# Performance work log

Hardware: AMD Instinct MI355X
Metric: run time of the kernel (lower is better)

The kernel has to match this reference:

```python
import jax, jax.numpy as jnp
import numpy as np

N_NODES = 50000
N_EDGES = 800000
D_IN, D_HID, D_OUT = 128, 256, 128


def setup_inputs() -> dict:
    key = jax.random.key(0)
    ks = jax.random.split(key, 8)
    x = jax.random.normal(ks[0], (N_NODES, D_IN), dtype=jnp.float32)
    edge_index = jax.random.randint(ks[1], (2, N_EDGES), 0, N_NODES, dtype=jnp.int64)
    # Xavier-ish scale for stability
    W_l1 = jax.random.normal(ks[2], (D_HID, D_IN), dtype=jnp.float32) * (1.0 / np.sqrt(D_IN))
    b_l1 = jnp.zeros((D_HID,), dtype=jnp.float32)
    W_r1 = jax.random.normal(ks[3], (D_HID, D_IN), dtype=jnp.float32) * (1.0 / np.sqrt(D_IN))
    W_l2 = jax.random.normal(ks[4], (D_OUT, D_HID), dtype=jnp.float32) * (1.0 / np.sqrt(D_HID))
    b_l2 = jnp.zeros((D_OUT,), dtype=jnp.float32)
    W_r2 = jax.random.normal(ks[5], (D_OUT, D_HID), dtype=jnp.float32) * (1.0 / np.sqrt(D_HID))
    return {"x": x, "edge_index": edge_index, "W_l1": W_l1, "b_l1": b_l1,
            "W_r1": W_r1, "W_l2": W_l2, "b_l2": b_l2, "W_r2": W_r2}


def _sage_conv(x, src, dst, W_l, b_l, W_r):
    # SAGEConv (aggr='mean', root_weight=True, normalize=False):
    #   out_i = W_l @ mean_{j in N(i)} x_j + b_l + W_r @ x_i
    n = x.shape[0]
    msgs = x[src]                                             # [E, d] gather
    agg = jax.ops.segment_sum(msgs, dst, num_segments=n)      # [N, d] scatter-add
    deg = jax.ops.segment_sum(jnp.ones((src.shape[0],), x.dtype), dst,
                              num_segments=n)
    agg = agg / jnp.maximum(deg, 1.0)[:, None]                # mean (0 for isolated)
    return agg @ W_l.T + b_l + x @ W_r.T


def reference(x, edge_index, W_l1, b_l1, W_r1, W_l2, b_l2, W_r2):
    # Note: PyG BasicGNN with num_layers=1 and jk=None applies NO activation
    # after its single conv, so the stack is two bare SAGEConv layers.
    src, dst = edge_index[0], edge_index[1]
    h = _sage_conv(x, src, dst, W_l1, b_l1, W_r1)
    out = _sage_conv(h, src, dst, W_l2, b_l2, W_r2)
    return out
```

## Files before the change

kernel.cpp:

```cpp
#include <hip/hip_runtime.h>

typedef __attribute__((ext_vector_type(4))) float f32x4;
typedef __attribute__((ext_vector_type(8))) short bf16x8;

__device__ inline ushort f2bf(float f) {
    uint u = __builtin_bit_cast(uint, f);
    u += 0x7fff + ((u >> 16) & 1);
    return (ushort)(u >> 16);
}
__device__ inline float bf2f(ushort h) {
    uint u = ((uint)h) << 16;
    return __builtin_bit_cast(float, u);
}
__device__ inline uint packbf(float lo, float hi) {
    return (uint)f2bf(lo) | ((uint)f2bf(hi) << 16);
}

#define GRP 8
#define NSLICE 6250
#define CHUNK 2048

__global__ __launch_bounds__(256) void k_pre(
    const float* __restrict__ x,
    const float* __restrict__ Wl1, const float* __restrict__ Wr1,
    const float* __restrict__ Wl2, const float* __restrict__ Wr2,
    const int* __restrict__ ei,
    ushort* __restrict__ A1, ushort* __restrict__ W1cat, ushort* __restrict__ W2cat,
    int* __restrict__ cnt, int n, int nE, int nxb, int histBase)
{
    const int b = blockIdx.x;
    if (b < nxb) {
        int e4 = b * 256 + threadIdx.x;
        if (e4 >= n * 32) return;
        int i = e4 >> 5, c4 = e4 & 31;
        float4 v = *(const float4*)(x + (size_t)i * 128 + c4 * 4);
        ushort4 o;
        o.x = f2bf(v.x); o.y = f2bf(v.y); o.z = f2bf(v.z); o.w = f2bf(v.w);
        *(ushort4*)(A1 + (size_t)i * 256 + 128 + c4 * 4) = o;
        return;
    }
    if (b < nxb + 128) {
        int t = (b - nxb) * 256 + threadIdx.x;
        int which = t >> 14;
        int r = (t >> 6) & 255;
        int kq = t & 63;
        const float* src;
        ushort* dst;
        if (which == 0) {
            src = (kq < 32) ? (Wl1 + (size_t)r * 128 + kq * 4)
                            : (Wr1 + (size_t)r * 128 + (kq - 32) * 4);
            dst = W1cat + (size_t)r * 256 + kq * 4;
        } else {
            src = (r < 128) ? (Wl2 + (size_t)r * 256 + kq * 4)
                            : (Wr2 + (size_t)(r - 128) * 256 + kq * 4);
            dst = W2cat + (size_t)r * 256 + kq * 4;
        }
        float4 v = *(const float4*)src;
        ushort4 o;
        o.x = f2bf(v.x); o.y = f2bf(v.y); o.z = f2bf(v.z); o.w = f2bf(v.w);
        *(ushort4*)dst = o;
        return;
    }
    if (b < histBase) return;
    const int hb = b - histBase;
    const int g = hb & 7;
    const int c = hb >> 3;
    const int lo = g * NSLICE, hi = lo + NSLICE;
    #pragma unroll
    for (int p = 0; p < CHUNK / 256; ++p) {
        int e = c * CHUNK + p * 256 + threadIdx.x;
        if (e < nE) {
            int d = ei[nE + e];
            if (d >= lo && d < hi) atomicAdd(&cnt[d], 1);
        }
    }
}

__global__ __launch_bounds__(1024) void k_scan1(const int* __restrict__ cnt,
                                                int* __restrict__ rp,
                                                int* __restrict__ bsum, int n) {
    __shared__ int buf[1024];
    const int tid = threadIdx.x;
    const int i = blockIdx.x * 1024 + tid;
    int v = (i < n) ? cnt[i] : 0;
    buf[tid] = v;
    __syncthreads();
    #pragma unroll
    for (int off = 1; off < 1024; off <<= 1) {
        int t = 0;
        if (tid >= off) t = buf[tid - off];
        __syncthreads();
        if (tid >= off) buf[tid] += t;
        __syncthreads();
    }
    if (i < n) rp[i] = buf[tid] - v;
    if (tid == 1023) bsum[blockIdx.x] = buf[1023];
}

__global__ __launch_bounds__(1024) void k_scan3b(int* __restrict__ rp,
                                                 const int* __restrict__ bsum,
                                                 int nb, int n) {
    __shared__ int sofs;
    if (threadIdx.x < 64) {
        int i = threadIdx.x;
        int v = (i < nb) ? bsum[i] : 0;
        int s = v;
        #pragma unroll
        for (int off = 1; off < 64; off <<= 1) {
            int t = __shfl_up(s, off, 64);
            if (i >= off) s += t;
        }
        if (i == (int)blockIdx.x) sofs = s - v;
        if ((int)blockIdx.x == nb - 1 && i == nb - 1) rp[n] = s;
    }
    __syncthreads();
    int i = blockIdx.x * 1024 + threadIdx.x;
    if (i < n) rp[i] += sofs;
}

__global__ __launch_bounds__(256) void k_fill_p(const int* __restrict__ ei,
                                                const int* __restrict__ rp,
                                                int* __restrict__ cur,
                                                int* __restrict__ srt, int nE) {
    const int g = blockIdx.x & 7;
    const int c = blockIdx.x >> 3;
    const int lo = g * NSLICE, hi = lo + NSLICE;
    #pragma unroll
    for (int p = 0; p < CHUNK / 256; ++p) {
        int e = c * CHUNK + p * 256 + threadIdx.x;
        if (e < nE) {
            int d = ei[nE + e];
            if (d >= lo && d < hi) {
                int s = ei[e];
                int pos = rp[d] + atomicAdd(&cur[d], 1);
                srt[pos] = s;
            }
        }
    }
}

__global__ __launch_bounds__(256) void k_gather1(ushort* A1,
                                                 const int* __restrict__ srt,
                                                 const int* __restrict__ rp, int n) {
    const int node = blockIdx.x * 4 + (threadIdx.x >> 6);
    if (node >= n) return;
    const int lane = threadIdx.x & 63;
    const int quad = lane >> 4;
    const int col16 = (lane & 15) * 16;
    const int beg = rp[node], end = rp[node + 1];
    float a0 = 0.f, a1 = 0.f, a2 = 0.f, a3 = 0.f;
    float a4 = 0.f, a5 = 0.f, a6 = 0.f, a7 = 0.f;
    for (int e = beg; e < end; e += 16) {
        uint4 v[4]; int live[4];
        #pragma unroll
        for (int q = 0; q < 4; ++q) {
            int idx = e + q * 4 + quad;
            live[q] = idx < end;
            int s = srt[live[q] ? idx : end - 1];
            v[q] = *(const uint4*)((const char*)A1 + (size_t)s * 512 + 256 + col16);
        }
        #pragma unroll
        for (int q = 0; q < 4; ++q) {
            if (live[q]) {
                a0 += bf2f((ushort)v[q].x);  a1 += bf2f((ushort)(v[q].x >> 16));
                a2 += bf2f((ushort)v[q].y);  a3 += bf2f((ushort)(v[q].y >> 16));
                a4 += bf2f((ushort)v[q].z);  a5 += bf2f((ushort)(v[q].z >> 16));
                a6 += bf2f((ushort)v[q].w);  a7 += bf2f((ushort)(v[q].w >> 16));
            }
        }
    }
    a0 += __shfl_xor(a0, 16); a1 += __shfl_xor(a1, 16);
    a2 += __shfl_xor(a2, 16); a3 += __shfl_xor(a3, 16);
    a4 += __shfl_xor(a4, 16); a5 += __shfl_xor(a5, 16);
    a6 += __shfl_xor(a6, 16); a7 += __shfl_xor(a7, 16);
    a0 += __shfl_xor(a0, 32); a1 += __shfl_xor(a1, 32);
    a2 += __shfl_xor(a2, 32); a3 += __shfl_xor(a3, 32);
    a4 += __shfl_xor(a4, 32); a5 += __shfl_xor(a5, 32);
    a6 += __shfl_xor(a6, 32); a7 += __shfl_xor(a7, 32);
    if (quad == 0) {
        const float invd = 1.0f / fmaxf((float)(end - beg), 1.0f);
        uint4 o;
        o.x = packbf(a0 * invd, a1 * invd);
        o.y = packbf(a2 * invd, a3 * invd);
        o.z = packbf(a4 * invd, a5 * invd);
        o.w = packbf(a6 * invd, a7 * invd);
        *(uint4*)((char*)A1 + (size_t)node * 512 + col16) = o;
    }
}

__global__ __launch_bounds__(256) void k_gather2(const ushort* __restrict__ H2,
                                                 const int* __restrict__ srt,
                                                 const int* __restrict__ rp,
                                                 const float* __restrict__ b2,
                                                 float* __restrict__ out, int n) {
    const int node = blockIdx.x * 4 + (threadIdx.x >> 6);
    if (node >= n) return;
    const int lane = threadIdx.x & 63;
    const int quad = lane >> 4;
    const int col16 = (lane & 15) * 16;
    const int beg = rp[node], end = rp[node + 1];
    float a0 = 0.f, a1 = 0.f, a2 = 0.f, a3 = 0.f;
    float a4 = 0.f, a5 = 0.f, a6 = 0.f, a7 = 0.f;
    for (int e = beg; e < end; e += 16) {
        uint4 v[4]; int live[4];
        #pragma unroll
        for (int q = 0; q < 4; ++q) {
            int idx = e + q * 4 + quad;
            live[q] = idx < end;
            int s = srt[live[q] ? idx : end - 1];
            v[q] = *(const uint4*)((const char*)H2 + (size_t)s * 512 + col16);
        }
        #pragma unroll
        for (int q = 0; q < 4; ++q) {
            if (live[q]) {
                a0 += bf2f((ushort)v[q].x);  a1 += bf2f((ushort)(v[q].x >> 16));
                a2 += bf2f((ushort)v[q].y);  a3 += bf2f((ushort)(v[q].y >> 16));
                a4 += bf2f((ushort)v[q].z);  a5 += bf2f((ushort)(v[q].z >> 16));
                a6 += bf2f((ushort)v[q].w);  a7 += bf2f((ushort)(v[q].w >> 16));
            }
        }
    }
    a0 += __shfl_xor(a0, 16); a1 += __shfl_xor(a1, 16);
    a2 += __shfl_xor(a2, 16); a3 += __shfl_xor(a3, 16);
    a4 += __shfl_xor(a4, 16); a5 += __shfl_xor(a5, 16);
    a6 += __shfl_xor(a6, 16); a7 += __shfl_xor(a7, 16);
    a0 += __shfl_xor(a0, 32); a1 += __shfl_xor(a1, 32);
    a2 += __shfl_xor(a2, 32); a3 += __shfl_xor(a3, 32);
    a4 += __shfl_xor(a4, 32); a5 += __shfl_xor(a5, 32);
    a6 += __shfl_xor(a6, 32); a7 += __shfl_xor(a7, 32);
    if (quad == 0) {
        const float invd = 1.0f / fmaxf((float)(end - beg), 1.0f);
        uint4 rv = *(const uint4*)((const char*)H2 + (size_t)node * 512 + 256 + col16);
        const int c8 = (lane & 15) * 8;
        float4 bb0 = *(const float4*)(b2 + c8);
        float4 bb1 = *(const float4*)(b2 + c8 + 4);
        float4 r0, r1;
        r0.x = a0 * invd + bf2f((ushort)rv.x) + bb0.x;
        r0.y = a1 * invd + bf2f((ushort)(rv.x >> 16)) + bb0.y;
        r0.z = a2 * invd + bf2f((ushort)rv.y) + bb0.z;
        r0.w = a3 * invd + bf2f((ushort)(rv.y >> 16)) + bb0.w;
        r1.x = a4 * invd + bf2f((ushort)rv.z) + bb1.x;
        r1.y = a5 * invd + bf2f((ushort)(rv.z >> 16)) + bb1.y;
        r1.z = a6 * invd + bf2f((ushort)rv.w) + bb1.z;
        r1.w = a7 * invd + bf2f((ushort)(rv.w >> 16)) + bb1.w;
        *(float4*)(out + (size_t)node * 128 + c8) = r0;
        *(float4*)(out + (size_t)node * 128 + c8 + 4) = r1;
    }
}

__global__ __launch_bounds__(512, 6) void k_gemm_fused(
    const ushort* __restrict__ A, const ushort* __restrict__ W1,
    const ushort* __restrict__ W2, const float* __restrict__ b1,
    ushort* __restrict__ O, int n)
{
    __shared__ __align__(16) char sA[32768];
    const int bi = blockIdx.x * 64;
    const int tid = threadIdx.x;

    #pragma unroll
    for (int p = 0; p < 4; ++p) {
        const int o = p * 8192 + tid * 16;
        const int row = o >> 9;
        const int cb = o & 511;
        uint4 v = *(const uint4*)((const char*)A + (size_t)(bi + row) * 512 + cb);
        *(uint4*)(sA + row * 512 + (cb ^ ((row & 7) << 4))) = v;
    }
    __syncthreads();

    const int wid = tid >> 6;
    const int lane = tid & 63;
    const int wn = wid * 32;
    const int lr = lane & 15;
    const int lkb = (lane >> 4) * 16;
    const int crow0 = (lane >> 4) * 4;
    const int ccol = lane & 15;

    f32x4 acc[4][2] = {};
    #pragma unroll
    for (int kk = 0; kk < 8; ++kk) {
        bf16x8 wf[2], af[4];
        #pragma unroll
        for (int ni = 0; ni < 2; ++ni)
            wf[ni] = *(const bf16x8*)((const char*)W1 + (size_t)(wn + ni * 16 + lr) * 512 + kk * 64 + lkb);
        #pragma unroll
        for (int mi = 0; mi < 4; ++mi) {
            const int row = mi * 16 + lr;
            af[mi] = *(const bf16x8*)(sA + row * 512 + ((kk * 64 + lkb) ^ ((row & 7) << 4)));
        }
        #pragma unroll
        for (int mi = 0; mi < 4; ++mi)
            #pragma unroll
            for (int ni = 0; ni < 2; ++ni)
                acc[mi][ni] = __builtin_amdgcn_mfma_f32_16x16x32_bf16(
                    af[mi], wf[ni], acc[mi][ni], 0, 0, 0);
    }
    __syncthreads();

    {
        const float badd0 = b1[wn + ccol];
        const float badd1 = b1[wn + 16 + ccol];
        #pragma unroll
        for (int mi = 0; mi < 4; ++mi)
            #pragma unroll
            for (int ni = 0; ni < 2; ++ni) {
                const int col = wn + ni * 16 + ccol;
                const float badd = ni ? badd1 : badd0;
                #pragma unroll
                for (int j = 0; j < 4; ++j) {
                    const int row = mi * 16 + crow0 + j;
                    *(ushort*)(sA + row * 512 + ((col * 2) ^ ((row & 7) << 4))) =
                        f2bf(acc[mi][ni][j] + badd);
                }
            }
    }
    __syncthreads();

    {
        f32x4 acc2[4][2] = {};
        #pragma unroll
        for (int kk = 0; kk < 8; ++kk) {
            bf16x8 wf[2], af[4];
            #pragma unroll
            for (int ni = 0; ni < 2; ++ni)
                wf[ni] = *(const bf16x8*)((const char*)W2 + (size_t)(wn + ni * 16 + lr) * 512 + kk * 64 + lkb);
            #pragma unroll
            for (int mi = 0; mi < 4; ++mi) {
                const int row = mi * 16 + lr;
                af[mi] = *(const bf16x8*)(sA + row * 512 + ((kk * 64 + lkb) ^ ((row & 7) << 4)));
            }
            #pragma unroll
            for (int mi = 0; mi < 4; ++mi)
                #pragma unroll
                for (int ni = 0; ni < 2; ++ni)
                    acc2[mi][ni] = __builtin_amdgcn_mfma_f32_16x16x32_bf16(
                        af[mi], wf[ni], acc2[mi][ni], 0, 0, 0);
        }
        #pragma unroll
        for (int mi = 0; mi < 4; ++mi)
            #pragma unroll
            for (int ni = 0; ni < 2; ++ni) {
                const int ocol = wn + ni * 16 + ccol;
                #pragma unroll
                for (int j = 0; j < 4; ++j) {
                    const int grow = bi + mi * 16 + crow0 + j;
                    if (grow < n)
                        O[(size_t)grow * 256 + ocol] = f2bf(acc2[mi][ni][j]);
                }
            }
    }
}

extern "C" void kernel_launch(void* const* d_in, const int* in_sizes, int n_in,
                              void* d_out, int out_size, void* d_ws, size_t ws_size,
                              hipStream_t stream) {
    const float* x   = (const float*)d_in[0];
    const int*   ei  = (const int*)  d_in[1];
    const float* Wl1 = (const float*)d_in[2];
    const float* bl1 = (const float*)d_in[3];
    const float* Wr1 = (const float*)d_in[4];
    const float* Wl2 = (const float*)d_in[5];
    const float* bl2 = (const float*)d_in[6];
    const float* Wr2 = (const float*)d_in[7];
    float* out = (float*)d_out;

    const int nN = 50000;
    const int nE = in_sizes[1] / 2;

    char* ws = (char*)d_ws;
    int*    rp    = (int*)   (ws);
    int*    cnt   = (int*)   (ws + 262144);
    int*    cur   = (int*)   (ws + 524288);
    int*    bsum  = (int*)   (ws + 786432);
    int*    srt   = (int*)   (ws + (size_t)1 * (1 << 20));
    ushort* W1cat = (ushort*)(ws + (size_t)5 * (1 << 20));
    ushort* W2cat = (ushort*)(ws + (size_t)5 * (1 << 20) + 262144);
    ushort* A1    = (ushort*)(ws + (size_t)6 * (1 << 20));
    ushort* H2    = (ushort*)(ws + (size_t)32 * (1 << 20));

    const int nb = (nN + 1023) / 1024;
    const int nChunks = (nE + CHUNK - 1) / CHUNK;
    const int nxb = (nN * 32 + 255) / 256;
    const int histBase = (nxb + 128 + 7) & ~7;

    hipMemsetAsync(cnt, 0, 524288, stream);

    k_pre<<<histBase + nChunks * GRP, 256, 0, stream>>>(
        x, Wl1, Wr1, Wl2, Wr2, ei, A1, W1cat, W2cat, cnt, nN, nE, nxb, histBase);

    k_scan1<<<nb, 1024, 0, stream>>>(cnt, rp, bsum, nN);
    k_scan3b<<<nb, 1024, 0, stream>>>(rp, bsum, nb, nN);
    k_fill_p<<<nChunks * GRP, 256, 0, stream>>>(ei, rp, cur, srt, nE);

    k_gather1<<<(nN + 3) / 4, 256, 0, stream>>>(A1, srt, rp, nN);
    k_gemm_fused<<<(nN + 63) / 64, 512, 0, stream>>>(A1, W1cat, W2cat, bl1, H2, nN);
    k_gather2<<<(nN + 3) / 4, 256, 0, stream>>>(H2, srt, rp, bl2, out, nN);
}
```

Before: 269.7 us.

## Fuse layer-1 neighbor gather into the fused GEMM kernel and split outputs

The first-layer mean aggregation is now done inside the GEMM kernel. Each block gathers neighbor rows for its 64 nodes straight into shared memory, which removes the separate gather kernel and the round trip of the aggregated half of A1 through global memory. The bf16 copy of x is stored compactly (128 columns) and the second GEMM's outputs go to separate T2 and Rb buffers, so gathers read denser rows. W1 and W2 fragments are preloaded into registers, which raises register pressure; the launch_bounds occupancy hint is dropped and the gather runs at lower parallelism, only 8 waves per 64 nodes.

```diff
diff --git a/kernel.cpp b/kernel.cpp
--- a/kernel.cpp
+++ b/kernel.cpp
@@ -25,7 +25,7 @@
     const float* __restrict__ Wl1, const float* __restrict__ Wr1,
     const float* __restrict__ Wl2, const float* __restrict__ Wr2,
     const int* __restrict__ ei,
-    ushort* __restrict__ A1, ushort* __restrict__ W1cat, ushort* __restrict__ W2cat,
+    ushort* __restrict__ A1x, ushort* __restrict__ W1cat, ushort* __restrict__ W2cat,
     int* __restrict__ cnt, int n, int nE, int nxb, int histBase)
 {
     const int b = blockIdx.x;
@@ -36,7 +36,7 @@
         float4 v = *(const float4*)(x + (size_t)i * 128 + c4 * 4);
         ushort4 o;
         o.x = f2bf(v.x); o.y = f2bf(v.y); o.z = f2bf(v.z); o.w = f2bf(v.w);
-        *(ushort4*)(A1 + (size_t)i * 256 + 128 + c4 * 4) = o;
+        *(ushort4*)(A1x + (size_t)i * 128 + c4 * 4) = o;
         return;
     }
     if (b < nxb + 128) {
@@ -139,56 +139,170 @@
     }
 }
 
-__global__ __launch_bounds__(256) void k_gather1(ushort* A1,
-                                                 const int* __restrict__ srt,
-                                                 const int* __restrict__ rp, int n) {
-    const int node = blockIdx.x * 4 + (threadIdx.x >> 6);
-    if (node >= n) return;
-    const int lane = threadIdx.x & 63;
+__global__ __launch_bounds__(512) void k_gemm_fused(
+    const ushort* __restrict__ A1x, const ushort* __restrict__ W1,
+    const ushort* __restrict__ W2, const float* __restrict__ b1,
+    const int* __restrict__ srt, const int* __restrict__ rp,
+    ushort* __restrict__ T2, ushort* __restrict__ Rb, int n)
+{
+    __shared__ __align__(16) char sA[32768];
+    const int bi = blockIdx.x * 64;
+    const int tid = threadIdx.x;
+    const int wid = tid >> 6;
+    const int lane = tid & 63;
+    const int wn = wid * 32;
+    const int lr = lane & 15;
+    const int lkb = (lane >> 4) * 16;
     const int quad = lane >> 4;
     const int col16 = (lane & 15) * 16;
-    const int beg = rp[node], end = rp[node + 1];
-    float a0 = 0.f, a1 = 0.f, a2 = 0.f, a3 = 0.f;
-    float a4 = 0.f, a5 = 0.f, a6 = 0.f, a7 = 0.f;
-    for (int e = beg; e < end; e += 16) {
-        uint4 v[4]; int live[4];
-        #pragma unroll
-        for (int q = 0; q < 4; ++q) {
-            int idx = e + q * 4 + quad;
-            live[q] = idx < end;
-            int s = srt[live[q] ? idx : end - 1];
-            v[q] = *(const uint4*)((const char*)A1 + (size_t)s * 512 + 256 + col16);
-        }
-        #pragma unroll
-        for (int q = 0; q < 4; ++q) {
-            if (live[q]) {
-                a0 += bf2f((ushort)v[q].x);  a1 += bf2f((ushort)(v[q].x >> 16));
-                a2 += bf2f((ushort)v[q].y);  a3 += bf2f((ushort)(v[q].y >> 16));
-                a4 += bf2f((ushort)v[q].z);  a5 += bf2f((ushort)(v[q].z >> 16));
-                a6 += bf2f((ushort)v[q].w);  a7 += bf2f((ushort)(v[q].w >> 16));
-            }
-        }
-    }
-    a0 += __shfl_xor(a0, 16); a1 += __shfl_xor(a1, 16);
-    a2 += __shfl_xor(a2, 16); a3 += __shfl_xor(a3, 16);
-    a4 += __shfl_xor(a4, 16); a5 += __shfl_xor(a5, 16);
-    a6 += __shfl_xor(a6, 16); a7 += __shfl_xor(a7, 16);
-    a0 += __shfl_xor(a0, 32); a1 += __shfl_xor(a1, 32);
-    a2 += __shfl_xor(a2, 32); a3 += __shfl_xor(a3, 32);
-    a4 += __shfl_xor(a4, 32); a5 += __shfl_xor(a5, 32);
-    a6 += __shfl_xor(a6, 32); a7 += __shfl_xor(a7, 32);
-    if (quad == 0) {
-        const float invd = 1.0f / fmaxf((float)(end - beg), 1.0f);
-        uint4 o;
-        o.x = packbf(a0 * invd, a1 * invd);
-        o.y = packbf(a2 * invd, a3 * invd);
-        o.z = packbf(a4 * invd, a5 * invd);
-        o.w = packbf(a6 * invd, a7 * invd);
-        *(uint4*)((char*)A1 + (size_t)node * 512 + col16) = o;
-    }
-}
-
-__global__ __launch_bounds__(256) void k_gather2(const ushort* __restrict__ H2,
+
+    bf16x8 w1r[16];
+    #pragma unroll
+    for (int kk = 0; kk < 8; ++kk)
+        #pragma unroll
+        for (int ni = 0; ni < 2; ++ni)
+            w1r[kk * 2 + ni] = *(const bf16x8*)((const char*)W1 +
+                (size_t)(wn + ni * 16 + lr) * 512 + kk * 64 + lkb);
+
+    #pragma unroll
+    for (int p = 0; p < 2; ++p) {
+        const int idx = p * 512 + tid;
+        const int row = idx >> 4;
+        const int cb = (idx & 15) * 16;
+        uint4 v = *(const uint4*)((const char*)A1x + (size_t)(bi + row) * 256 + cb);
+        *(uint4*)(sA + row * 512 + ((256 + cb) ^ ((row & 7) << 4))) = v;
+    }
+
+    #pragma unroll 1
+    for (int i = 0; i < 8; ++i) {
+        const int row = wid * 8 + i;
+        const int node = bi + row;
+        if (node >= n) continue;
+        const int beg = rp[node], end = rp[node + 1];
+        float a0 = 0.f, a1 = 0.f, a2 = 0.f, a3 = 0.f;
+        float a4 = 0.f, a5 = 0.f, a6 = 0.f, a7 = 0.f;
+        for (int e = beg; e < end; e += 16) {
+            uint4 v[4]; int live[4];
+            #pragma unroll
+            for (int q = 0; q < 4; ++q) {
+                int idx = e + q * 4 + quad;
+                live[q] = idx < end;
+                int s = srt[live[q] ? idx : end - 1];
+                v[q] = *(const uint4*)((const char*)A1x + (size_t)s * 256 + col16);
+            }
+            #pragma unroll
+            for (int q = 0; q < 4; ++q) {
+                if (live[q]) {
+                    a0 += bf2f((ushort)v[q].x);  a1 += bf2f((ushort)(v[q].x >> 16));
+                    a2 += bf2f((ushort)v[q].y);  a3 += bf2f((ushort)(v[q].y >> 16));
+                    a4 += bf2f((ushort)v[q].z);  a5 += bf2f((ushort)(v[q].z >> 16));
+                    a6 += bf2f((ushort)v[q].w);  a7 += bf2f((ushort)(v[q].w >> 16));
+                }
+            }
+        }
+        a0 += __shfl_xor(a0, 16); a1 += __shfl_xor(a1, 16);
+        a2 += __shfl_xor(a2, 16); a3 += __shfl_xor(a3, 16);
+        a4 += __shfl_xor(a4, 16); a5 += __shfl_xor(a5, 16);
+        a6 += __shfl_xor(a6, 16); a7 += __shfl_xor(a7, 16);
+        a0 += __shfl_xor(a0, 32); a1 += __shfl_xor(a1, 32);
+        a2 += __shfl_xor(a2, 32); a3 += __shfl_xor(a3, 32);
+        a4 += __shfl_xor(a4, 32); a5 += __shfl_xor(a5, 32);
+        a6 += __shfl_xor(a6, 32); a7 += __shfl_xor(a7, 32);
+        if (quad == 0) {
+            const float invd = 1.0f / fmaxf((float)(end - beg), 1.0f);
+            uint4 o;
+            o.x = packbf(a0 * invd, a1 * invd);
+            o.y = packbf(a2 * invd, a3 * invd);
+            o.z = packbf(a4 * invd, a5 * invd);
+            o.w = packbf(a6 * invd, a7 * invd);
+            *(uint4*)(sA + row * 512 + (col16 ^ ((row & 7) << 4))) = o;
+        }
+    }
+    __syncthreads();
+
+    const int crow0 = (lane >> 4) * 4;
+    const int ccol = lane & 15;
+
+    f32x4 acc[4][2] = {};
+    {
+        bf16x8 w2r[16];
+        #pragma unroll
+        for (int kk = 0; kk < 8; ++kk)
+            #pragma unroll
+            for (int ni = 0; ni < 2; ++ni)
+                w2r[kk * 2 + ni] = *(const bf16x8*)((const char*)W2 +
+                    (size_t)(wn + ni * 16 + lr) * 512 + kk * 64 + lkb);
+
+        #pragma unroll
+        for (int kk = 0; kk < 8; ++kk) {
+            bf16x8 af[4];
+            #pragma unroll
+            for (int mi = 0; mi < 4; ++mi) {
+                const int row = mi * 16 + lr;
+                af[mi] = *(const bf16x8*)(sA + row * 512 + ((kk * 64 + lkb) ^ ((row & 7) << 4)));
+            }
+            #pragma unroll
+            for (int mi = 0; mi < 4; ++mi)
+                #pragma unroll
+                for (int ni = 0; ni < 2; ++ni)
+                    acc[mi][ni] = __builtin_amdgcn_mfma_f32_16x16x32_bf16(
+                        af[mi], w1r[kk * 2 + ni], acc[mi][ni], 0, 0, 0);
+        }
+        __syncthreads();
+
+        {
+            const float badd0 = b1[wn + ccol];
+            const float badd1 = b1[wn + 16 + ccol];
+            #pragma unroll
+            for (int mi = 0; mi < 4; ++mi)
+                #pragma unroll
+                for (int ni = 0; ni < 2; ++ni) {
+                    const int col = wn + ni * 16 + ccol;
+                    const float badd = ni ? badd1 : badd0;
+                    #pragma unroll
+                    for (int j = 0; j < 4; ++j) {
+                        const int row = mi * 16 + crow0 + j;
+                        *(ushort*)(sA + row * 512 + ((col * 2) ^ ((row & 7) << 4))) =
+                            f2bf(acc[mi][ni][j] + badd);
+                    }
+                }
+        }
+        __syncthreads();
+
+        f32x4 acc2[4][2] = {};
+        #pragma unroll
+        for (int kk = 0; kk < 8; ++kk) {
+            bf16x8 af[4];
+            #pragma unroll
+            for (int mi = 0; mi < 4; ++mi) {
+                const int row = mi * 16 + lr;
+                af[mi] = *(const bf16x8*)(sA + row * 512 + ((kk * 64 + lkb) ^ ((row & 7) << 4)));
+            }
+            #pragma unroll
+            for (int mi = 0; mi < 4; ++mi)
+                #pragma unroll
+                for (int ni = 0; ni < 2; ++ni)
+                    acc2[mi][ni] = __builtin_amdgcn_mfma_f32_16x16x32_bf16(
+                        af[mi], w2r[kk * 2 + ni], acc2[mi][ni], 0, 0, 0);
+        }
+        #pragma unroll
+        for (int mi = 0; mi < 4; ++mi)
+            #pragma unroll
+            for (int ni = 0; ni < 2; ++ni) {
+                const int ocol = wn + ni * 16 + ccol;
+                ushort* dstbase = (ocol < 128) ? (T2 + ocol) : (Rb + ocol - 128);
+                #pragma unroll
+                for (int j = 0; j < 4; ++j) {
+                    const int grow = bi + mi * 16 + crow0 + j;
+                    if (grow < n)
+                        dstbase[(size_t)grow * 128] = f2bf(acc2[mi][ni][j]);
+                }
+            }
+    }
+}
+
+__global__ __launch_bounds__(256) void k_gather2(const ushort* __restrict__ T2,
+                                                 const ushort* __restrict__ Rb,
                                                  const int* __restrict__ srt,
                                                  const int* __restrict__ rp,
                                                  const float* __restrict__ b2,
@@ -208,7 +322,7 @@
             int idx = e + q * 4 + quad;
             live[q] = idx < end;
             int s = srt[live[q] ? idx : end - 1];
-            v[q] = *(const uint4*)((const char*)H2 + (size_t)s * 512 + col16);
+            v[q] = *(const uint4*)((const char*)T2 + (size_t)s * 256 + col16);
         }
         #pragma unroll
         for (int q = 0; q < 4; ++q) {
@@ -230,7 +344,7 @@
     a6 += __shfl_xor(a6, 32); a7 += __shfl_xor(a7, 32);
     if (quad == 0) {
         const float invd = 1.0f / fmaxf((float)(end - beg), 1.0f);
-        uint4 rv = *(const uint4*)((const char*)H2 + (size_t)node * 512 + 256 + col16);
+        uint4 rv = *(const uint4*)((const char*)Rb + (size_t)node * 256 + col16);
         const int c8 = (lane & 15) * 8;
         float4 bb0 = *(const float4*)(b2 + c8);
         float4 bb1 = *(const float4*)(b2 + c8 + 4);
@@ -248,108 +362,6 @@
     }
 }
 
-__global__ __launch_bounds__(512, 6) void k_gemm_fused(
-    const ushort* __restrict__ A, const ushort* __restrict__ W1,
-    const ushort* __restrict__ W2, const float* __restrict__ b1,
-    ushort* __restrict__ O, int n)
-{
-    __shared__ __align__(16) char sA[32768];
-    const int bi = blockIdx.x * 64;
-    const int tid = threadIdx.x;
-
-    #pragma unroll
-    for (int p = 0; p < 4; ++p) {
-        const int o = p * 8192 + tid * 16;
-        const int row = o >> 9;
-        const int cb = o & 511;
-        uint4 v = *(const uint4*)((const char*)A + (size_t)(bi + row) * 512 + cb);
-        *(uint4*)(sA + row * 512 + (cb ^ ((row & 7) << 4))) = v;
-    }
-    __syncthreads();
-
-    const int wid = tid >> 6;
-    const int lane = tid & 63;
-    const int wn = wid * 32;
-    const int lr = lane & 15;
-    const int lkb = (lane >> 4) * 16;
-    const int crow0 = (lane >> 4) * 4;
-    const int ccol = lane & 15;
-
-    f32x4 acc[4][2] = {};
-    #pragma unroll
-    for (int kk = 0; kk < 8; ++kk) {
-        bf16x8 wf[2], af[4];
-        #pragma unroll
-        for (int ni = 0; ni < 2; ++ni)
-            wf[ni] = *(const bf16x8*)((const char*)W1 + (size_t)(wn + ni * 16 + lr) * 512 + kk * 64 + lkb);
-        #pragma unroll
-        for (int mi = 0; mi < 4; ++mi) {
-            const int row = mi * 16 + lr;
-            af[mi] = *(const bf16x8*)(sA + row * 512 + ((kk * 64 + lkb) ^ ((row & 7) << 4)));
-        }
-        #pragma unroll
-        for (int mi = 0; mi < 4; ++mi)
-            #pragma unroll
-            for (int ni = 0; ni < 2; ++ni)
-                acc[mi][ni] = __builtin_amdgcn_mfma_f32_16x16x32_bf16(
-                    af[mi], wf[ni], acc[mi][ni], 0, 0, 0);
-    }
-    __syncthreads();
-
-    {
-        const float badd0 = b1[wn + ccol];
-        const float badd1 = b1[wn + 16 + ccol];
-        #pragma unroll
-        for (int mi = 0; mi < 4; ++mi)
-            #pragma unroll
-            for (int ni = 0; ni < 2; ++ni) {
-                const int col = wn + ni * 16 + ccol;
-                const float badd = ni ? badd1 : badd0;
-                #pragma unroll
-                for (int j = 0; j < 4; ++j) {
-                    const int row = mi * 16 + crow0 + j;
-                    *(ushort*)(sA + row * 512 + ((col * 2) ^ ((row & 7) << 4))) =
-                        f2bf(acc[mi][ni][j] + badd);
-                }
-            }
-    }
-    __syncthreads();
-
-    {
-        f32x4 acc2[4][2] = {};
-        #pragma unroll
-        for (int kk = 0; kk < 8; ++kk) {
-            bf16x8 wf[2], af[4];
-            #pragma unroll
-            for (int ni = 0; ni < 2; ++ni)
-                wf[ni] = *(const bf16x8*)((const char*)W2 + (size_t)(wn + ni * 16 + lr) * 512 + kk * 64 + lkb);
-            #pragma unroll
-            for (int mi = 0; mi < 4; ++mi) {
-                const int row = mi * 16 + lr;
-                af[mi] = *(const bf16x8*)(sA + row * 512 + ((kk * 64 + lkb) ^ ((row & 7) << 4)));
-            }
-            #pragma unroll
-            for (int mi = 0; mi < 4; ++mi)
-                #pragma unroll
-                for (int ni = 0; ni < 2; ++ni)
-                    acc2[mi][ni] = __builtin_amdgcn_mfma_f32_16x16x32_bf16(
-                        af[mi], wf[ni], acc2[mi][ni], 0, 0, 0);
-        }
-        #pragma unroll
-        for (int mi = 0; mi < 4; ++mi)
-            #pragma unroll
-            for (int ni = 0; ni < 2; ++ni) {
-                const int ocol = wn + ni * 16 + ccol;
-                #pragma unroll
-                for (int j = 0; j < 4; ++j) {
-                    const int grow = bi + mi * 16 + crow0 + j;
-                    if (grow < n)
-                        O[(size_t)grow * 256 + ocol] = f2bf(acc2[mi][ni][j]);
-                }
-            }
-    }
-}
-
 extern "C" void kernel_launch(void* const* d_in, const int* in_sizes, int n_in,
                               void* d_out, int out_size, void* d_ws, size_t ws_size,
                               hipStream_t stream) {
@@ -374,8 +386,9 @@
     int*    srt   = (int*)   (ws + (size_t)1 * (1 << 20));
     ushort* W1cat = (ushort*)(ws + (size_t)5 * (1 << 20));
     ushort* W2cat = (ushort*)(ws + (size_t)5 * (1 << 20) + 262144);
-    ushort* A1    = (ushort*)(ws + (size_t)6 * (1 << 20));
-    ushort* H2    = (ushort*)(ws + (size_t)32 * (1 << 20));
+    ushort* A1x   = (ushort*)(ws + (size_t)6 * (1 << 20));
+    ushort* T2    = (ushort*)(ws + (size_t)20 * (1 << 20));
+    ushort* Rb    = (ushort*)(ws + (size_t)34 * (1 << 20));
 
     const int nb = (nN + 1023) / 1024;
     const int nChunks = (nE + CHUNK - 1) / CHUNK;
@@ -385,13 +398,14 @@
     hipMemsetAsync(cnt, 0, 524288, stream);
 
     k_pre<<<histBase + nChunks * GRP, 256, 0, stream>>>(
-        x, Wl1, Wr1, Wl2, Wr2, ei, A1, W1cat, W2cat, cnt, nN, nE, nxb, histBase);
+        x, Wl1, Wr1, Wl2, Wr2, ei, A1x, W1cat, W2cat, cnt, nN, nE, nxb, histBase);
 
     k_scan1<<<nb, 1024, 0, stream>>>(cnt, rp, bsum, nN);
     k_scan3b<<<nb, 1024, 0, stream>>>(rp, bsum, nb, nN);
     k_fill_p<<<nChunks * GRP, 256, 0, stream>>>(ei, rp, cur, srt, nE);
 
-    k_gather1<<<(nN + 3) / 4, 256, 0, stream>>>(A1, srt, rp, nN);
-    k_gemm_fused<<<(nN + 63) / 64, 512, 0, stream>>>(A1, W1cat, W2cat, bl1, H2, nN);
-    k_gather2<<<(nN + 3) / 4, 256, 0, stream>>>(H2, srt, rp, bl2, out, nN);
-}
+    k_gemm_fused<<<(nN + 63) / 64, 512, 0, stream>>>(
+        A1x, W1cat, W2cat, bl1, srt, rp, T2, Rb, nN);
+
+    k_gather2<<<(nN + 3) / 4, 256, 0, stream>>>(T2, Rb, srt, rp, bl2, out, nN);
+}
```

New measurement: 283.0 us. +5.0%, slower.

## Split gather waves across two nodes and widen fused GEMM tile with register-resident weights

Applied to the files above, without the earlier changes.

The gather kernels now let each 64-lane wave handle two nodes with 32 lanes each, which removes one cross-lane shuffle reduction and halves the grid size. This targets wasted lanes on low-degree nodes, where the average degree is 16. The fused two-layer GEMM now processes 128 rows per block instead of 64 and preloads the W1 and W2 fragments into registers once per block, so weights are no longer reloaded from global memory on every k step. This needs 64KB of LDS and many more registers, and lowers the occupancy hint to 2, which may reduce latency hiding.

```diff
diff --git a/kernel.cpp b/kernel.cpp
--- a/kernel.cpp
+++ b/kernel.cpp
@@ -142,19 +142,20 @@
 __global__ __launch_bounds__(256) void k_gather1(ushort* A1,
                                                  const int* __restrict__ srt,
                                                  const int* __restrict__ rp, int n) {
-    const int node = blockIdx.x * 4 + (threadIdx.x >> 6);
+    const int wav = blockIdx.x * 4 + (threadIdx.x >> 6);
+    const int lane = threadIdx.x & 63;
+    const int node = wav * 2 + (lane >> 5);
     if (node >= n) return;
-    const int lane = threadIdx.x & 63;
-    const int quad = lane >> 4;
+    const int q2 = (lane >> 4) & 1;
     const int col16 = (lane & 15) * 16;
     const int beg = rp[node], end = rp[node + 1];
     float a0 = 0.f, a1 = 0.f, a2 = 0.f, a3 = 0.f;
     float a4 = 0.f, a5 = 0.f, a6 = 0.f, a7 = 0.f;
-    for (int e = beg; e < end; e += 16) {
+    for (int e = beg; e < end; e += 8) {
         uint4 v[4]; int live[4];
         #pragma unroll
         for (int q = 0; q < 4; ++q) {
-            int idx = e + q * 4 + quad;
+            int idx = e + q * 2 + q2;
             live[q] = idx < end;
             int s = srt[live[q] ? idx : end - 1];
             v[q] = *(const uint4*)((const char*)A1 + (size_t)s * 512 + 256 + col16);
@@ -173,11 +174,7 @@
     a2 += __shfl_xor(a2, 16); a3 += __shfl_xor(a3, 16);
     a4 += __shfl_xor(a4, 16); a5 += __shfl_xor(a5, 16);
     a6 += __shfl_xor(a6, 16); a7 += __shfl_xor(a7, 16);
-    a0 += __shfl_xor(a0, 32); a1 += __shfl_xor(a1, 32);
-    a2 += __shfl_xor(a2, 32); a3 += __shfl_xor(a3, 32);
-    a4 += __shfl_xor(a4, 32); a5 += __shfl_xor(a5, 32);
-    a6 += __shfl_xor(a6, 32); a7 += __shfl_xor(a7, 32);
-    if (quad == 0) {
+    if (q2 == 0) {
         const float invd = 1.0f / fmaxf((float)(end - beg), 1.0f);
         uint4 o;
         o.x = packbf(a0 * invd, a1 * invd);
@@ -193,19 +190,20 @@
                                                  const int* __restrict__ rp,
                                                  const float* __restrict__ b2,
                                                  float* __restrict__ out, int n) {
-    const int node = blockIdx.x * 4 + (threadIdx.x >> 6);
+    const int wav = blockIdx.x * 4 + (threadIdx.x >> 6);
+    const int lane = threadIdx.x & 63;
+    const int node = wav * 2 + (lane >> 5);
     if (node >= n) return;
-    const int lane = threadIdx.x & 63;
-    const int quad = lane >> 4;
+    const int q2 = (lane >> 4) & 1;
     const int col16 = (lane & 15) * 16;
     const int beg = rp[node], end = rp[node + 1];
     float a0 = 0.f, a1 = 0.f, a2 = 0.f, a3 = 0.f;
     float a4 = 0.f, a5 = 0.f, a6 = 0.f, a7 = 0.f;
-    for (int e = beg; e < end; e += 16) {
+    for (int e = beg; e < end; e += 8) {
         uint4 v[4]; int live[4];
         #pragma unroll
         for (int q = 0; q < 4; ++q) {
-            int idx = e + q * 4 + quad;
+            int idx = e + q * 2 + q2;
             live[q] = idx < end;
             int s = srt[live[q] ? idx : end - 1];
             v[q] = *(const uint4*)((const char*)H2 + (size_t)s * 512 + col16);
@@ -224,11 +222,7 @@
     a2 += __shfl_xor(a2, 16); a3 += __shfl_xor(a3, 16);
     a4 += __shfl_xor(a4, 16); a5 += __shfl_xor(a5, 16);
     a6 += __shfl_xor(a6, 16); a7 += __shfl_xor(a7, 16);
-    a0 += __shfl_xor(a0, 32); a1 += __shfl_xor(a1, 32);
-    a2 += __shfl_xor(a2, 32); a3 += __shfl_xor(a3, 32);
-    a4 += __shfl_xor(a4, 32); a5 += __shfl_xor(a5, 32);
-    a6 += __shfl_xor(a6, 32); a7 += __shfl_xor(a7, 32);
-    if (quad == 0) {
+    if (q2 == 0) {
         const float invd = 1.0f / fmaxf((float)(end - beg), 1.0f);
         uint4 rv = *(const uint4*)((const char*)H2 + (size_t)node * 512 + 256 + col16);
         const int c8 = (lane & 15) * 8;
@@ -248,17 +242,30 @@
     }
 }
 
-__global__ __launch_bounds__(512, 6) void k_gemm_fused(
+__global__ __launch_bounds__(512, 2) void k_gemm(
     const ushort* __restrict__ A, const ushort* __restrict__ W1,
     const ushort* __restrict__ W2, const float* __restrict__ b1,
     ushort* __restrict__ O, int n)
 {
-    __shared__ __align__(16) char sA[32768];
-    const int bi = blockIdx.x * 64;
+    __shared__ __align__(16) char sA[65536];
+    const int bi = blockIdx.x * 128;
     const int tid = threadIdx.x;
-
-    #pragma unroll
-    for (int p = 0; p < 4; ++p) {
+    const int wid = tid >> 6;
+    const int lane = tid & 63;
+    const int wn = wid * 32;
+    const int lr = lane & 15;
+    const int lkb = (lane >> 4) * 16;
+
+    bf16x8 w1r[16];
+    #pragma unroll
+    for (int kk = 0; kk < 8; ++kk)
+        #pragma unroll
+        for (int ni = 0; ni < 2; ++ni)
+            w1r[kk * 2 + ni] = *(const bf16x8*)((const char*)W1 +
+                (size_t)(wn + ni * 16 + lr) * 512 + kk * 64 + lkb);
+
+    #pragma unroll
+    for (int p = 0; p < 8; ++p) {
         const int o = p * 8192 + tid * 16;
         const int row = o >> 9;
         const int cb = o & 511;
@@ -267,32 +274,29 @@
     }
     __syncthreads();
 
-    const int wid = tid >> 6;
-    const int lane = tid & 63;
-    const int wn = wid * 32;
-    const int lr = lane & 15;
-    const int lkb = (lane >> 4) * 16;
+    bf16x8 w2r[16];
+    #pragma unroll
+    for (int kk = 0; kk < 8; ++kk)
+        #pragma unroll
+        for (int ni = 0; ni < 2; ++ni)
+            w2r[kk * 2 + ni] = *(const bf16x8*)((const char*)W2 +
+                (size_t)(wn + ni * 16 + lr) * 512 + kk * 64 + lkb);
+
     const int crow0 = (lane >> 4) * 4;
     const int ccol = lane & 15;
 
-    f32x4 acc[4][2] = {};
+    f32x4 acc[8][2] = {};
     #pragma unroll
     for (int kk = 0; kk < 8; ++kk) {
-        bf16x8 wf[2], af[4];
-        #pragma unroll
-        for (int ni = 0; ni < 2; ++ni)
-            wf[ni] = *(const bf16x8*)((const char*)W1 + (size_t)(wn + ni * 16 + lr) * 512 + kk * 64 + lkb);
-        #pragma unroll
-        for (int mi = 0; mi < 4; ++mi) {
+        #pragma unroll
+        for (int mi = 0; mi < 8; ++mi) {
             const int row = mi * 16 + lr;
-            af[mi] = *(const bf16x8*)(sA + row * 512 + ((kk * 64 + lkb) ^ ((row & 7) << 4)));
-        }
-        #pragma unroll
-        for (int mi = 0; mi < 4; ++mi)
+            bf16x8 af = *(const bf16x8*)(sA + row * 512 + ((kk * 64 + lkb) ^ ((row & 7) << 4)));
             #pragma unroll
             for (int ni = 0; ni < 2; ++ni)
                 acc[mi][ni] = __builtin_amdgcn_mfma_f32_16x16x32_bf16(
-                    af[mi], wf[ni], acc[mi][ni], 0, 0, 0);
+                    af, w1r[kk * 2 + ni], acc[mi][ni], 0, 0, 0);
+        }
     }
     __syncthreads();
 
@@ -300,7 +304,7 @@
         const float badd0 = b1[wn + ccol];
         const float badd1 = b1[wn + 16 + ccol];
         #pragma unroll
-        for (int mi = 0; mi < 4; ++mi)
+        for (int mi = 0; mi < 8; ++mi)
             #pragma unroll
             for (int ni = 0; ni < 2; ++ni) {
                 const int col = wn + ni * 16 + ccol;
@@ -315,39 +319,35 @@
     }
     __syncthreads();
 
-    {
-        f32x4 acc2[4][2] = {};
-        #pragma unroll
-        for (int kk = 0; kk < 8; ++kk) {
-            bf16x8 wf[2], af[4];
+    #pragma unroll
+    for (int mi = 0; mi < 8; ++mi)
+        #pragma unroll
+        for (int ni = 0; ni < 2; ++ni)
+            acc[mi][ni] = (f32x4){0.f, 0.f, 0.f, 0.f};
+    #pragma unroll
+    for (int kk = 0; kk < 8; ++kk) {
+        #pragma unroll
+        for (int mi = 0; mi < 8; ++mi) {
+            const int row = mi * 16 + lr;
+            bf16x8 af = *(const bf16x8*)(sA + row * 512 + ((kk * 64 + lkb) ^ ((row & 7) << 4)));
             #pragma unroll
             for (int ni = 0; ni < 2; ++ni)
-                wf[ni] = *(const bf16x8*)((const char*)W2 + (size_t)(wn + ni * 16 + lr) * 512 + kk * 64 + lkb);
+                acc[mi][ni] = __builtin_amdgcn_mfma_f32_16x16x32_bf16(
+                    af, w2r[kk * 2 + ni], acc[mi][ni], 0, 0, 0);
+        }
+    }
+    #pragma unroll
+    for (int mi = 0; mi < 8; ++mi)
+        #pragma unroll
+        for (int ni = 0; ni < 2; ++ni) {
+            const int ocol = wn + ni * 16 + ccol;
             #pragma unroll
-            for (int mi = 0; mi < 4; ++mi) {
-                const int row = mi * 16 + lr;
-                af[mi] = *(const bf16x8*)(sA + row * 512 + ((kk * 64 + lkb) ^ ((row & 7) << 4)));
-            }
-            #pragma unroll
-            for (int mi = 0; mi < 4; ++mi)
-                #pragma unroll
-                for (int ni = 0; ni < 2; ++ni)
-                    acc2[mi][ni] = __builtin_amdgcn_mfma_f32_16x16x32_bf16(
-                        af[mi], wf[ni], acc2[mi][ni], 0, 0, 0);
-        }
-        #pragma unroll
-        for (int mi = 0; mi < 4; ++mi)
-            #pragma unroll
-            for (int ni = 0; ni < 2; ++ni) {
-                const int ocol = wn + ni * 16 + ccol;
-                #pragma unroll
-                for (int j = 0; j < 4; ++j) {
-                    const int grow = bi + mi * 16 + crow0 + j;
-                    if (grow < n)
-                        O[(size_t)grow * 256 + ocol] = f2bf(acc2[mi][ni][j]);
-                }
-            }
-    }
+            for (int j = 0; j < 4; ++j) {
+                const int grow = bi + mi * 16 + crow0 + j;
+                if (grow < n)
+                    O[(size_t)grow * 256 + ocol] = f2bf(acc[mi][ni][j]);
+            }
+        }
 }
 
 extern "C" void kernel_launch(void* const* d_in, const int* in_sizes, int n_in,
@@ -391,7 +391,7 @@
     k_scan3b<<<nb, 1024, 0, stream>>>(rp, bsum, nb, nN);
     k_fill_p<<<nChunks * GRP, 256, 0, stream>>>(ei, rp, cur, srt, nE);
 
-    k_gather1<<<(nN + 3) / 4, 256, 0, stream>>>(A1, srt, rp, nN);
-    k_gemm_fused<<<(nN + 63) / 64, 512, 0, stream>>>(A1, W1cat, W2cat, bl1, H2, nN);
-    k_gather2<<<(nN + 3) / 4, 256, 0, stream>>>(H2, srt, rp, bl2, out, nN);
-}
+    k_gather1<<<(nN + 7) / 8, 256, 0, stream>>>(A1, srt, rp, nN);
+    k_gemm<<<(nN + 127) / 128, 512, 0, stream>>>(A1, W1cat, W2cat, bl1, H2, nN);
+    k_gather2<<<(nN + 7) / 8, 256, 0, stream>>>(H2, srt, rp, bl2, out, nN);
+}
```

Result: faster. 261.4 us (-3.1%).
